# Kernel optimization log

Hardware: AMD Instinct MI355X
Metric: run time of the kernel (lower is better)

Reference implementation:

```python
import jax, jax.numpy as jnp
import numpy as np

EMBED = 768
HEADS = 12
HEAD_DIM = EMBED // HEADS
WINDOW_SIZES = (16, 64, 256)
LN_EPS = 1e-5


def setup_inputs() -> dict:
    key = jax.random.key(0)
    ks = jax.random.split(key, 8)
    B, S = 4, 1024
    s = 1.0 / np.sqrt(EMBED)
    return {
        "query": jax.random.normal(ks[0], (B, S, EMBED), dtype=jnp.float32),
        "key": jax.random.normal(ks[1], (B, S, EMBED), dtype=jnp.float32),
        "value": jax.random.normal(ks[2], (B, S, EMBED), dtype=jnp.float32),
        "attention_mask": jnp.ones((B, S), dtype=jnp.float32),
        "Wq": jax.random.normal(ks[3], (EMBED, EMBED), dtype=jnp.float32) * s,
        "bq": jnp.zeros((EMBED,), dtype=jnp.float32),
        "Wk": jax.random.normal(ks[4], (EMBED, EMBED), dtype=jnp.float32) * s,
        "bk": jnp.zeros((EMBED,), dtype=jnp.float32),
        "Wv": jax.random.normal(ks[5], (EMBED, EMBED), dtype=jnp.float32) * s,
        "bv": jnp.zeros((EMBED,), dtype=jnp.float32),
        "window_weights": jnp.ones((len(WINDOW_SIZES),), dtype=jnp.float32) / len(WINDOW_SIZES),
        "gamma": jnp.ones((EMBED,), dtype=jnp.float32),
        "beta": jnp.zeros((EMBED,), dtype=jnp.float32),
    }


def reference(query, key, value, attention_mask, Wq, bq, Wk, bk, Wv, bv,
              window_weights, gamma, beta):
    B, S, _ = query.shape

    def proj(x, W, b):
        # [B,S,E] -> [B,H,S,D]  (torch nn.Linear: x @ W.T + b)
        return (x @ W.T + b).reshape(B, S, HEADS, HEAD_DIM).transpose(0, 2, 1, 3)

    q = proj(query, Wq, bq)
    k = proj(key, Wk, bk)
    v = proj(value, Wv, bv)

    # full [B,H,S,S] scores (dropout in eval mode = identity)
    scores = jnp.einsum("bhqd,bhkd->bhqk", q, k) / np.sqrt(HEAD_DIM)

    idx = jnp.arange(S)
    am = attention_mask[:, None, None, :]  # broadcast over heads and query dim
    combined = jnp.zeros_like(scores)
    for i, w in enumerate(WINDOW_SIZES):
        # band mask |i-j| <= w; note scores are multiplicatively masked
        # and carried across scales, exactly as in the torch loop
        band = (jnp.abs(idx[:, None] - idx[None, :]) <= w).astype(scores.dtype)
        scores = scores * band * am
        combined = combined + window_weights[i] * jax.nn.softmax(scores, axis=-1)

    context = jnp.einsum("bhqk,bhkd->bhqd", combined, v)
    context = context.transpose(0, 2, 1, 3).reshape(B, S, EMBED)
    q_flat = q.transpose(0, 2, 1, 3).reshape(B, S, EMBED)

    x = q_flat + context
    mean = jnp.mean(x, axis=-1, keepdims=True)
    var = jnp.var(x, axis=-1, keepdims=True)
    return gamma * (x - mean) / jnp.sqrt(var + LN_EPS) + beta
```

## Files before the change

### kernel.cpp

```cpp
#include <hip/hip_runtime.h>
#include <hip/hip_bf16.h>

#define EMB   768
#define SEQ   1024
#define NBAT  4
#define MROWS 4096
#define NHEAD 12
#define HD    64
#define WIN   16
#define QB    16
#define KB    64
#define LN_EPS 1e-5f

typedef __attribute__((ext_vector_type(8))) short bf16x8;
typedef __attribute__((ext_vector_type(4))) float f32x4;
typedef unsigned short u16;
typedef unsigned int   u32;

static __device__ inline u16 f2bf(float f) {
    union { float f; u32 u; } a; a.f = f;
    u32 u = a.u;
    u32 r = (u + 0x7fffu + ((u >> 16) & 1u)) >> 16;
    return (u16)r;
}
static __device__ inline float bf2f(u16 x) {
    union { u32 u; float f; } c; c.u = ((u32)x) << 16; return c.f;
}

#define ACT4 786432u
#define WT4  147456u
__global__ __launch_bounds__(256) void cast_all(
    const float* __restrict__ q, const float* __restrict__ k, const float* __restrict__ v,
    const float* __restrict__ wq, const float* __restrict__ wk, const float* __restrict__ wv,
    u16* __restrict__ Abf, u16* __restrict__ Wbf)
{
    u32 u = blockIdx.x * 256u + threadIdx.x;
    const float* src; u16* dst; u32 off;
    if (u < 3u * ACT4) {
        u32 which = u / ACT4;
        off = (u - which * ACT4) * 4u;
        src = which == 0 ? q : (which == 1 ? k : v);
        dst = Abf + (size_t)which * 3145728u + off;
    } else {
        u32 w2 = u - 3u * ACT4;
        u32 which = w2 / WT4;
        off = (w2 - which * WT4) * 4u;
        src = which == 0 ? wq : (which == 1 ? wk : wv);
        dst = Wbf + (size_t)which * 589824u + off;
    }
    float4 val = *(const float4*)(src + off);
    ushort4 o;
    o.x = f2bf(val.x); o.y = f2bf(val.y); o.z = f2bf(val.z); o.w = f2bf(val.w);
    *(ushort4*)dst = o;
}

#define GK 768
#define GN 768

static __device__ inline void gload_lds16(const void* g, void* l) {
    __builtin_amdgcn_global_load_lds((const __attribute__((address_space(1))) void*)g,
                                     (__attribute__((address_space(3))) void*)l, 16, 0, 0);
}

__global__ __launch_bounds__(256) void gemm_qkv(
    const u16* __restrict__ Abase, const u16* __restrict__ Wbase,
    const float* __restrict__ bq, const float* __restrict__ bk, const float* __restrict__ bv,
    u16* __restrict__ Qb, u16* __restrict__ Kb, u16* __restrict__ Vb)
{
    const int z = blockIdx.z;
    const u16* A = Abase + (size_t)z * (MROWS * GK);
    const u16* W = Wbase + (size_t)z * (GN * GK);
    const float* bias = (z == 0) ? bq : ((z == 1) ? bk : bv);
    u16* Ob = (z == 0) ? Qb : ((z == 1) ? Kb : Vb);

    int id = blockIdx.y * 6 + blockIdx.x;
    int swz = (id & 7) * 48 + (id >> 3);
    const int bm = (swz / 6) * 64, bn = (swz % 6) * 128;

    const int tid = threadIdx.x, wave = tid >> 6, lane = tid & 63;

    __shared__ __align__(16) u16 As[2][64 * 64];
    __shared__ __align__(16) u16 Bs[2][128 * 64];

    f32x4 acc[2][4];
#pragma unroll
    for (int i = 0; i < 2; ++i)
#pragma unroll
        for (int j = 0; j < 4; ++j) acc[i][j] = (f32x4){0.f, 0.f, 0.f, 0.f};

    const int wr = (wave >> 1) * 32, wc = (wave & 1) * 64;
    const int r0 = lane & 15, hk = lane >> 4;

    int arow[2], acol[2], brow[4], bcol[4];
#pragma unroll
    for (int j = 0; j < 2; ++j) {
        int c = j * 256 + tid;
        arow[j] = c >> 3;
        acol[j] = ((c & 7) ^ (arow[j] & 7)) * 8;
    }
#pragma unroll
    for (int j = 0; j < 4; ++j) {
        int c = j * 256 + tid;
        brow[j] = c >> 3;
        bcol[j] = ((c & 7) ^ (brow[j] & 7)) * 8;
    }

#define GEMM_STAGE(buf, K0) do { \
    _Pragma("unroll") for (int j = 0; j < 2; ++j) \
        gload_lds16(A + (size_t)(bm + arow[j]) * GK + (K0) + acol[j], \
                    &As[buf][(j * 256 + wave * 64) * 8]); \
    _Pragma("unroll") for (int j = 0; j < 4; ++j) \
        gload_lds16(W + (size_t)(bn + brow[j]) * GK + (K0) + bcol[j], \
                    &Bs[buf][(j * 256 + wave * 64) * 8]); \
} while (0)

#define GEMM_COMPUTE(buf) do { \
    bf16x8 af[2][2], bg[2][4]; \
    _Pragma("unroll") for (int kk = 0; kk < 2; ++kk) { \
        _Pragma("unroll") for (int i = 0; i < 2; ++i) { \
            int ra = wr + i * 16 + r0; int sa = (kk * 4 + hk) ^ (ra & 7); \
            af[kk][i] = *(const bf16x8*)&As[buf][ra * 64 + sa * 8]; } \
        _Pragma("unroll") for (int j = 0; j < 4; ++j) { \
            int rb = wc + j * 16 + r0; int sb = (kk * 4 + hk) ^ (rb & 7); \
            bg[kk][j] = *(const bf16x8*)&Bs[buf][rb * 64 + sb * 8]; } } \
    _Pragma("unroll") for (int kk = 0; kk < 2; ++kk) \
    _Pragma("unroll") for (int i = 0; i < 2; ++i) \
    _Pragma("unroll") for (int j = 0; j < 4; ++j) \
        acc[i][j] = __builtin_amdgcn_mfma_f32_16x16x32_bf16(af[kk][i], bg[kk][j], acc[i][j], 0, 0, 0); \
} while (0)

    GEMM_STAGE(0, 0);
    for (int t = 0; t < 11; ++t) {
        int cur = t & 1;
        GEMM_STAGE(cur ^ 1, (t + 1) * 64);
        asm volatile("s_waitcnt vmcnt(6)" ::: "memory");
        __builtin_amdgcn_sched_barrier(0);
        __builtin_amdgcn_s_barrier();
        __builtin_amdgcn_sched_barrier(0);
        GEMM_COMPUTE(cur);
        __builtin_amdgcn_sched_barrier(0);
        __builtin_amdgcn_s_barrier();
        __builtin_amdgcn_sched_barrier(0);
    }
    asm volatile("s_waitcnt vmcnt(0)" ::: "memory");
    __builtin_amdgcn_sched_barrier(0);
    __builtin_amdgcn_s_barrier();
    __builtin_amdgcn_sched_barrier(0);
    GEMM_COMPUTE(1);

#undef GEMM_STAGE
#undef GEMM_COMPUTE

    const int cl = lane & 15, rb4 = (lane >> 4) * 4;
#pragma unroll
    for (int i = 0; i < 2; ++i)
#pragma unroll
        for (int j = 0; j < 4; ++j) {
            int col = bn + wc + j * 16 + cl;
            float b_ = bias[col];
#pragma unroll
            for (int r = 0; r < 4; ++r) {
                int row = bm + wr + i * 16 + rb4 + r;
                Ob[(size_t)row * GN + col] = f2bf(acc[i][j][r] + b_);
            }
        }
}

__global__ __launch_bounds__(256) void vsum_kernel(const u16* __restrict__ Vb, float* __restrict__ Vsum)
{
    const int b = blockIdx.y;
    const int l = threadIdx.x & 63, sg = threadIdx.x >> 6;
    const int e = blockIdx.x * 64 + l;
    float s = 0.f;
    const u16* p = Vb + ((size_t)b * SEQ + sg * 256) * EMB + e;
    for (int r = 0; r < 256; ++r) s += bf2f(p[(size_t)r * EMB]);
    __shared__ float red[4][64];
    red[sg][l] = s;
    __syncthreads();
    if (sg == 0) Vsum[b * EMB + e] = red[0][l] + red[1][l] + red[2][l] + red[3][l];
}

__global__ __launch_bounds__(768, 3) void attn_ln(
    const u16* __restrict__ Qb, const u16* __restrict__ Kb, const u16* __restrict__ Vb,
    const float* __restrict__ Vsum, const float* __restrict__ am, const float* __restrict__ ww,
    const float* __restrict__ gamma, const float* __restrict__ beta, float* __restrict__ out)
{
    int id = blockIdx.x + 64 * blockIdx.y;
    int swz = (id & 7) * 32 + (id >> 3);
    const int qt = swz & 63, b = swz >> 6;

    const int q0 = qt * QB;
    int kstart = q0 - WIN;
    if (kstart < 0) kstart = 0;
    if (kstart > SEQ - KB) kstart = SEQ - KB;

    const int h = threadIdx.x >> 6, lane = threadIdx.x & 63;
    const int fr = lane & 15, hk = lane >> 4;
    const int kof = hk * 8, rowg = hk * 4;

    __shared__ __align__(16) u16 Ps[NHEAD][QB][68];
    __shared__ float ps1[QB][13], ps2[QB][13];
    __shared__ float mu[QB], rs[QB];

    const float w0 = ww[0], w1 = ww[1], w2 = ww[2];

    bf16x8 aq[2], bk4[4][2], bv4[4][2];
    {
        const u16* qb = Qb + ((size_t)(b * SEQ + q0)) * EMB + h * HD;
#pragma unroll
        for (int kk = 0; kk < 2; ++kk)
            aq[kk] = *(const bf16x8*)(qb + (size_t)fr * EMB + kk * 32 + kof);
        const u16* kb = Kb + ((size_t)(b * SEQ + kstart)) * EMB + h * HD;
#pragma unroll
        for (int nj = 0; nj < 4; ++nj)
#pragma unroll
            for (int kk = 0; kk < 2; ++kk)
                bk4[nj][kk] = *(const bf16x8*)(kb + (size_t)(nj * 16 + fr) * EMB + kk * 32 + kof);
        const u16* vb = Vb + ((size_t)(b * SEQ + kstart)) * EMB + h * HD;
#pragma unroll
        for (int nj = 0; nj < 4; ++nj)
#pragma unroll
            for (int kk = 0; kk < 2; ++kk) {
                union { bf16x8 v; u16 s[8]; } tmp;
#pragma unroll
                for (int j = 0; j < 8; ++j)
                    tmp.s[j] = vb[(size_t)(kk * 32 + kof + j) * EMB + nj * 16 + fr];
                bv4[nj][kk] = tmp.v;
            }
    }

    f32x4 sc[4];
#pragma unroll
    for (int j = 0; j < 4; ++j) sc[j] = (f32x4){0.f, 0.f, 0.f, 0.f};
#pragma unroll
    for (int kk = 0; kk < 2; ++kk)
#pragma unroll
        for (int nj = 0; nj < 4; ++nj)
            sc[nj] = __builtin_amdgcn_mfma_f32_16x16x32_bf16(aq[kk], bk4[nj][kk], sc[nj], 0, 0, 0);

    float amv[4];
#pragma unroll
    for (int nj = 0; nj < 4; ++nj) amv[nj] = am[b * SEQ + kstart + nj * 16 + fr];

    float t[4][4], cj[4][4], ua[4];
#pragma unroll
    for (int nj = 0; nj < 4; ++nj)
#pragma unroll
        for (int r = 0; r < 4; ++r) {
            int qrow = q0 + rowg + r;
            int kcol = kstart + nj * 16 + fr;
            int d = qrow - kcol; if (d < 0) d = -d;
            t[nj][r] = (d <= WIN) ? sc[nj][r] * 0.125f * amv[nj] : 0.f;
            cj[nj][r] = 0.f;
        }
#pragma unroll
    for (int r = 0; r < 4; ++r) ua[r] = 0.f;

#pragma unroll
    for (int it = 0; it < 3; ++it) {
        float wwi = it == 0 ? w0 : (it == 1 ? w1 : w2);
#pragma unroll
        for (int r = 0; r < 4; ++r) {
            float m = 0.f;
#pragma unroll
            for (int nj = 0; nj < 4; ++nj) m = fmaxf(m, t[nj][r]);
#pragma unroll
            for (int o = 1; o < 16; o <<= 1) m = fmaxf(m, __shfl_xor(m, o, 64));
            float e4[4], s = 0.f;
#pragma unroll
            for (int nj = 0; nj < 4; ++nj) { e4[nj] = __expf(t[nj][r] - m); s += e4[nj]; }
#pragma unroll
            for (int o = 1; o < 16; o <<= 1) s += __shfl_xor(s, o, 64);
            float un = __expf(-m);
            s += (float)(SEQ - KB) * un;
            float inv = wwi / s;
#pragma unroll
            for (int nj = 0; nj < 4; ++nj) cj[nj][r] += e4[nj] * inv;
            ua[r] += un * inv;
        }
        if (it < 2) {
#pragma unroll
            for (int nj = 0; nj < 4; ++nj)
#pragma unroll
                for (int r = 0; r < 4; ++r) t[nj][r] *= amv[nj];
        }
    }

#pragma unroll
    for (int nj = 0; nj < 4; ++nj)
#pragma unroll
        for (int r = 0; r < 4; ++r)
            Ps[h][rowg + r][nj * 16 + fr] = f2bf(cj[nj][r] - ua[r]);

    f32x4 pv[4];
#pragma unroll
    for (int j = 0; j < 4; ++j) pv[j] = (f32x4){0.f, 0.f, 0.f, 0.f};
#pragma unroll
    for (int kk = 0; kk < 2; ++kk) {
        bf16x8 ap = *(const bf16x8*)&Ps[h][fr][kk * 32 + kof];
#pragma unroll
        for (int nj = 0; nj < 4; ++nj)
            pv[nj] = __builtin_amdgcn_mfma_f32_16x16x32_bf16(ap, bv4[nj][kk], pv[nj], 0, 0, 0);
    }

    float vs[4];
#pragma unroll
    for (int nj = 0; nj < 4; ++nj) vs[nj] = Vsum[b * EMB + h * HD + nj * 16 + fr];

    float xv[4][4];
#pragma unroll
    for (int nj = 0; nj < 4; ++nj)
#pragma unroll
        for (int r = 0; r < 4; ++r) {
            int row = q0 + rowg + r;
            float qres = bf2f(Qb[((size_t)(b * SEQ + row)) * EMB + h * HD + nj * 16 + fr]);
            xv[nj][r] = qres + pv[nj][r] + ua[r] * vs[nj];
        }

    float s1r[4], s2r[4];
#pragma unroll
    for (int r = 0; r < 4; ++r) {
        float a = 0.f, c = 0.f;
#pragma unroll
        for (int nj = 0; nj < 4; ++nj) { a += xv[nj][r]; c += xv[nj][r] * xv[nj][r]; }
#pragma unroll
        for (int o = 1; o < 16; o <<= 1) { a += __shfl_xor(a, o, 64); c += __shfl_xor(c, o, 64); }
        s1r[r] = a; s2r[r] = c;
    }
    if (fr == 0) {
#pragma unroll
        for (int r = 0; r < 4; ++r) { ps1[rowg + r][h] = s1r[r]; ps2[rowg + r][h] = s2r[r]; }
    }
    __syncthreads();
    if (h == 0 && lane < QB) {
        float a = 0.f, c = 0.f;
#pragma unroll
        for (int w = 0; w < NHEAD; ++w) { a += ps1[lane][w]; c += ps2[lane][w]; }
        float mean = a * (1.f / EMB);
        float var = c * (1.f / EMB) - mean * mean;
        mu[lane] = mean;
        rs[lane] = rsqrtf(var + LN_EPS);
    }
    __syncthreads();

#pragma unroll
    for (int nj = 0; nj < 4; ++nj) {
        int col = h * HD + nj * 16 + fr;
        float g = gamma[col], be = beta[col];
#pragma unroll
        for (int r = 0; r < 4; ++r) {
            int row = q0 + rowg + r;
            out[((size_t)(b * SEQ + row)) * EMB + col] =
                g * (xv[nj][r] - mu[rowg + r]) * rs[rowg + r] + be;
        }
    }
}

extern "C" void kernel_launch(void* const* d_in, const int* in_sizes, int n_in,
                              void* d_out, int out_size, void* d_ws, size_t ws_size,
                              hipStream_t stream)
{
    const float* q     = (const float*)d_in[0];
    const float* k     = (const float*)d_in[1];
    const float* v     = (const float*)d_in[2];
    const float* amask = (const float*)d_in[3];
    const float* Wq    = (const float*)d_in[4];
    const float* bq    = (const float*)d_in[5];
    const float* Wk    = (const float*)d_in[6];
    const float* bk    = (const float*)d_in[7];
    const float* Wv    = (const float*)d_in[8];
    const float* bv    = (const float*)d_in[9];
    const float* ww    = (const float*)d_in[10];
    const float* gamma = (const float*)d_in[11];
    const float* beta  = (const float*)d_in[12];
    float* out = (float*)d_out;

    char* ws = (char*)d_ws;
    u16*   Abf  = (u16*)(ws);
    u16*   Wbf  = (u16*)(ws + 18874368);
    u16*   Qbf  = (u16*)(ws + 22413312);
    u16*   Kbf  = (u16*)(ws + 28704768);
    u16*   Vbf  = (u16*)(ws + 34996224);
    float* Vsum = (float*)(ws + 41287680);

    hipLaunchKernelGGL(cast_all, dim3(10944), dim3(256), 0, stream,
                       q, k, v, Wq, Wk, Wv, Abf, Wbf);
    hipLaunchKernelGGL(gemm_qkv, dim3(GN / 128, MROWS / 64, 3), dim3(256), 0, stream,
                       Abf, Wbf, bq, bk, bv, Qbf, Kbf, Vbf);
    hipLaunchKernelGGL(vsum_kernel, dim3(EMB / 64, NBAT), dim3(256), 0, stream,
                       Vbf, Vsum);
    hipLaunchKernelGGL(attn_ln, dim3(SEQ / QB, NBAT), dim3(768), 0, stream,
                       Qbf, Kbf, Vbf, Vsum, amask, ww, gamma, beta, out);
}
```

Before: 65.97 us.

## Fuse activation bf16 cast into QKV GEMM and pre-transpose V for attention

Drops the separate cast pass over the fp32 query/key/value activations. The GEMM now loads fp32 A fragments straight from global memory into registers, converts them to bf16 and feeds MFMA directly, while W still goes through LDS via async loads. The vsum kernel also writes a transposed copy of V so the attention kernel can load V fragments with vector loads instead of strided scalar gathers. The trade-offs are twice the A-side global bytes per GEMM block, no LDS reuse of A across waves, and an extra V-sized write.

```diff
diff --git a/kernel.cpp b/kernel.cpp
--- a/kernel.cpp
+++ b/kernel.cpp
@@ -26,32 +26,30 @@
 static __device__ inline float bf2f(u16 x) {
     union { u32 u; float f; } c; c.u = ((u32)x) << 16; return c.f;
 }
-
-#define ACT4 786432u
+static __device__ inline u32 cvt2(float lo, float hi) {
+    __hip_bfloat162 t = __float22bfloat162_rn(float2{lo, hi});
+    union { __hip_bfloat162 h; u32 u; } c; c.h = t; return c.u;
+}
+static __device__ inline bf16x8 pack8(float4 a, float4 b) {
+    union { bf16x8 v; u32 w[4]; } r;
+    r.w[0] = cvt2(a.x, a.y); r.w[1] = cvt2(a.z, a.w);
+    r.w[2] = cvt2(b.x, b.y); r.w[3] = cvt2(b.z, b.w);
+    return r.v;
+}
+
 #define WT4  147456u
-__global__ __launch_bounds__(256) void cast_all(
-    const float* __restrict__ q, const float* __restrict__ k, const float* __restrict__ v,
+__global__ __launch_bounds__(256) void cast_w(
     const float* __restrict__ wq, const float* __restrict__ wk, const float* __restrict__ wv,
-    u16* __restrict__ Abf, u16* __restrict__ Wbf)
+    u16* __restrict__ Wbf)
 {
     u32 u = blockIdx.x * 256u + threadIdx.x;
-    const float* src; u16* dst; u32 off;
-    if (u < 3u * ACT4) {
-        u32 which = u / ACT4;
-        off = (u - which * ACT4) * 4u;
-        src = which == 0 ? q : (which == 1 ? k : v);
-        dst = Abf + (size_t)which * 3145728u + off;
-    } else {
-        u32 w2 = u - 3u * ACT4;
-        u32 which = w2 / WT4;
-        off = (w2 - which * WT4) * 4u;
-        src = which == 0 ? wq : (which == 1 ? wk : wv);
-        dst = Wbf + (size_t)which * 589824u + off;
-    }
+    u32 which = u / WT4;
+    u32 off = (u - which * WT4) * 4u;
+    const float* src = which == 0 ? wq : (which == 1 ? wk : wv);
     float4 val = *(const float4*)(src + off);
     ushort4 o;
     o.x = f2bf(val.x); o.y = f2bf(val.y); o.z = f2bf(val.z); o.w = f2bf(val.w);
-    *(ushort4*)dst = o;
+    *(ushort4*)(Wbf + (size_t)which * 589824u + off) = o;
 }
 
 #define GK 768
@@ -63,12 +61,13 @@
 }
 
 __global__ __launch_bounds__(256) void gemm_qkv(
-    const u16* __restrict__ Abase, const u16* __restrict__ Wbase,
+    const float* __restrict__ qa, const float* __restrict__ ka, const float* __restrict__ va,
+    const u16* __restrict__ Wbase,
     const float* __restrict__ bq, const float* __restrict__ bk, const float* __restrict__ bv,
     u16* __restrict__ Qb, u16* __restrict__ Kb, u16* __restrict__ Vb)
 {
     const int z = blockIdx.z;
-    const u16* A = Abase + (size_t)z * (MROWS * GK);
+    const float* Af = (z == 0) ? qa : ((z == 1) ? ka : va);
     const u16* W = Wbase + (size_t)z * (GN * GK);
     const float* bias = (z == 0) ? bq : ((z == 1) ? bk : bv);
     u16* Ob = (z == 0) ? Qb : ((z == 1) ? Kb : Vb);
@@ -79,7 +78,6 @@
 
     const int tid = threadIdx.x, wave = tid >> 6, lane = tid & 63;
 
-    __shared__ __align__(16) u16 As[2][64 * 64];
     __shared__ __align__(16) u16 Bs[2][128 * 64];
 
     f32x4 acc[2][4];
@@ -90,14 +88,12 @@
 
     const int wr = (wave >> 1) * 32, wc = (wave & 1) * 64;
     const int r0 = lane & 15, hk = lane >> 4;
-
-    int arow[2], acol[2], brow[4], bcol[4];
-#pragma unroll
-    for (int j = 0; j < 2; ++j) {
-        int c = j * 256 + tid;
-        arow[j] = c >> 3;
-        acol[j] = ((c & 7) ^ (arow[j] & 7)) * 8;
-    }
+    const int fr = r0, kof = hk * 8;
+
+    const float* a0 = Af + (size_t)(bm + wr + fr) * GK + kof;
+    const float* a1 = a0 + 16 * GK;
+
+    int brow[4], bcol[4];
 #pragma unroll
     for (int j = 0; j < 4; ++j) {
         int c = j * 256 + tid;
@@ -105,35 +101,53 @@
         bcol[j] = ((c & 7) ^ (brow[j] & 7)) * 8;
     }
 
-#define GEMM_STAGE(buf, K0) do { \
-    _Pragma("unroll") for (int j = 0; j < 2; ++j) \
-        gload_lds16(A + (size_t)(bm + arow[j]) * GK + (K0) + acol[j], \
-                    &As[buf][(j * 256 + wave * 64) * 8]); \
+    float4 raw[2][2][2];
+    bf16x8 afrag[2][2];
+
+#define B_STAGE(buf, K0) do { \
     _Pragma("unroll") for (int j = 0; j < 4; ++j) \
         gload_lds16(W + (size_t)(bn + brow[j]) * GK + (K0) + bcol[j], \
                     &Bs[buf][(j * 256 + wave * 64) * 8]); \
 } while (0)
 
+#define ARAW(T) do { int kb = (T) * 64; \
+    raw[0][0][0] = *(const float4*)(a0 + kb);      raw[0][0][1] = *(const float4*)(a0 + kb + 4); \
+    raw[0][1][0] = *(const float4*)(a0 + kb + 32); raw[0][1][1] = *(const float4*)(a0 + kb + 36); \
+    raw[1][0][0] = *(const float4*)(a1 + kb);      raw[1][0][1] = *(const float4*)(a1 + kb + 4); \
+    raw[1][1][0] = *(const float4*)(a1 + kb + 32); raw[1][1][1] = *(const float4*)(a1 + kb + 36); \
+} while (0)
+
+#define ACVT() do { \
+    _Pragma("unroll") for (int kk = 0; kk < 2; ++kk) \
+    _Pragma("unroll") for (int i = 0; i < 2; ++i) \
+        afrag[kk][i] = pack8(raw[i][kk][0], raw[i][kk][1]); \
+} while (0)
+
 #define GEMM_COMPUTE(buf) do { \
-    bf16x8 af[2][2], bg[2][4]; \
-    _Pragma("unroll") for (int kk = 0; kk < 2; ++kk) { \
-        _Pragma("unroll") for (int i = 0; i < 2; ++i) { \
-            int ra = wr + i * 16 + r0; int sa = (kk * 4 + hk) ^ (ra & 7); \
-            af[kk][i] = *(const bf16x8*)&As[buf][ra * 64 + sa * 8]; } \
-        _Pragma("unroll") for (int j = 0; j < 4; ++j) { \
-            int rb = wc + j * 16 + r0; int sb = (kk * 4 + hk) ^ (rb & 7); \
-            bg[kk][j] = *(const bf16x8*)&Bs[buf][rb * 64 + sb * 8]; } } \
+    bf16x8 bg[2][4]; \
+    _Pragma("unroll") for (int kk = 0; kk < 2; ++kk) \
+    _Pragma("unroll") for (int j = 0; j < 4; ++j) { \
+        int rb = wc + j * 16 + r0; int sb = (kk * 4 + hk) ^ (rb & 7); \
+        bg[kk][j] = *(const bf16x8*)&Bs[buf][rb * 64 + sb * 8]; } \
     _Pragma("unroll") for (int kk = 0; kk < 2; ++kk) \
     _Pragma("unroll") for (int i = 0; i < 2; ++i) \
     _Pragma("unroll") for (int j = 0; j < 4; ++j) \
-        acc[i][j] = __builtin_amdgcn_mfma_f32_16x16x32_bf16(af[kk][i], bg[kk][j], acc[i][j], 0, 0, 0); \
+        acc[i][j] = __builtin_amdgcn_mfma_f32_16x16x32_bf16(afrag[kk][i], bg[kk][j], acc[i][j], 0, 0, 0); \
 } while (0)
 
-    GEMM_STAGE(0, 0);
-    for (int t = 0; t < 11; ++t) {
+    B_STAGE(0, 0);
+    ARAW(0);
+    for (int t = 0; t < 12; ++t) {
         int cur = t & 1;
-        GEMM_STAGE(cur ^ 1, (t + 1) * 64);
-        asm volatile("s_waitcnt vmcnt(6)" ::: "memory");
+        if (t < 11) {
+            B_STAGE(cur ^ 1, (t + 1) * 64);
+            asm volatile("s_waitcnt vmcnt(4)" ::: "memory");
+        } else {
+            asm volatile("s_waitcnt vmcnt(0)" ::: "memory");
+        }
+        __builtin_amdgcn_sched_barrier(0);
+        ACVT();
+        if (t < 11) ARAW(t + 1);
         __builtin_amdgcn_sched_barrier(0);
         __builtin_amdgcn_s_barrier();
         __builtin_amdgcn_sched_barrier(0);
@@ -142,13 +156,10 @@
         __builtin_amdgcn_s_barrier();
         __builtin_amdgcn_sched_barrier(0);
     }
-    asm volatile("s_waitcnt vmcnt(0)" ::: "memory");
-    __builtin_amdgcn_sched_barrier(0);
-    __builtin_amdgcn_s_barrier();
-    __builtin_amdgcn_sched_barrier(0);
-    GEMM_COMPUTE(1);
-
-#undef GEMM_STAGE
+
+#undef B_STAGE
+#undef ARAW
+#undef ACVT
 #undef GEMM_COMPUTE
 
     const int cl = lane & 15, rb4 = (lane >> 4) * 4;
@@ -166,14 +177,26 @@
         }
 }
 
-__global__ __launch_bounds__(256) void vsum_kernel(const u16* __restrict__ Vb, float* __restrict__ Vsum)
+__global__ __launch_bounds__(256) void vsum_kernel(const u16* __restrict__ Vb,
+                                                   float* __restrict__ Vsum,
+                                                   u16* __restrict__ Vt)
 {
     const int b = blockIdx.y;
     const int l = threadIdx.x & 63, sg = threadIdx.x >> 6;
     const int e = blockIdx.x * 64 + l;
     float s = 0.f;
     const u16* p = Vb + ((size_t)b * SEQ + sg * 256) * EMB + e;
-    for (int r = 0; r < 256; ++r) s += bf2f(p[(size_t)r * EMB]);
+    u16* vt = Vt + ((size_t)(b * EMB + e)) * SEQ + sg * 256;
+    for (int r8 = 0; r8 < 32; ++r8) {
+        union { bf16x8 v; u16 s8[8]; } buf;
+#pragma unroll
+        for (int j = 0; j < 8; ++j) {
+            u16 val = p[(size_t)(r8 * 8 + j) * EMB];
+            s += bf2f(val);
+            buf.s8[j] = val;
+        }
+        *(bf16x8*)(vt + r8 * 8) = buf.v;
+    }
     __shared__ float red[4][64];
     red[sg][l] = s;
     __syncthreads();
@@ -181,7 +204,7 @@
 }
 
 __global__ __launch_bounds__(768, 3) void attn_ln(
-    const u16* __restrict__ Qb, const u16* __restrict__ Kb, const u16* __restrict__ Vb,
+    const u16* __restrict__ Qb, const u16* __restrict__ Kb, const u16* __restrict__ Vt,
     const float* __restrict__ Vsum, const float* __restrict__ am, const float* __restrict__ ww,
     const float* __restrict__ gamma, const float* __restrict__ beta, float* __restrict__ out)
 {
@@ -216,17 +239,12 @@
 #pragma unroll
             for (int kk = 0; kk < 2; ++kk)
                 bk4[nj][kk] = *(const bf16x8*)(kb + (size_t)(nj * 16 + fr) * EMB + kk * 32 + kof);
-        const u16* vb = Vb + ((size_t)(b * SEQ + kstart)) * EMB + h * HD;
+        const u16* vt = Vt + ((size_t)(b * EMB + h * HD)) * SEQ + kstart;
 #pragma unroll
         for (int nj = 0; nj < 4; ++nj)
 #pragma unroll
-            for (int kk = 0; kk < 2; ++kk) {
-                union { bf16x8 v; u16 s[8]; } tmp;
-#pragma unroll
-                for (int j = 0; j < 8; ++j)
-                    tmp.s[j] = vb[(size_t)(kk * 32 + kof + j) * EMB + nj * 16 + fr];
-                bv4[nj][kk] = tmp.v;
-            }
+            for (int kk = 0; kk < 2; ++kk)
+                bv4[nj][kk] = *(const bf16x8*)(vt + (size_t)(nj * 16 + fr) * SEQ + kk * 32 + kof);
     }
 
     f32x4 sc[4];
@@ -376,19 +394,19 @@
     float* out = (float*)d_out;
 
     char* ws = (char*)d_ws;
-    u16*   Abf  = (u16*)(ws);
-    u16*   Wbf  = (u16*)(ws + 18874368);
-    u16*   Qbf  = (u16*)(ws + 22413312);
-    u16*   Kbf  = (u16*)(ws + 28704768);
-    u16*   Vbf  = (u16*)(ws + 34996224);
-    float* Vsum = (float*)(ws + 41287680);
-
-    hipLaunchKernelGGL(cast_all, dim3(10944), dim3(256), 0, stream,
-                       q, k, v, Wq, Wk, Wv, Abf, Wbf);
+    u16*   Wbf  = (u16*)(ws);
+    u16*   Qbf  = (u16*)(ws + 3538944);
+    u16*   Kbf  = (u16*)(ws + 9830400);
+    u16*   Vbf  = (u16*)(ws + 16121856);
+    u16*   Vt   = (u16*)(ws + 22413312);
+    float* Vsum = (float*)(ws + 28704768);
+
+    hipLaunchKernelGGL(cast_w, dim3(1728), dim3(256), 0, stream,
+                       Wq, Wk, Wv, Wbf);
     hipLaunchKernelGGL(gemm_qkv, dim3(GN / 128, MROWS / 64, 3), dim3(256), 0, stream,
-                       Abf, Wbf, bq, bk, bv, Qbf, Kbf, Vbf);
+                       q, k, v, Wbf, bq, bk, bv, Qbf, Kbf, Vbf);
     hipLaunchKernelGGL(vsum_kernel, dim3(EMB / 64, NBAT), dim3(256), 0, stream,
-                       Vbf, Vsum);
+                       Vbf, Vsum, Vt);
     hipLaunchKernelGGL(attn_ln, dim3(SEQ / QB, NBAT), dim3(768), 0, stream,
-                       Qbf, Kbf, Vbf, Vsum, amask, ww, gamma, beta, out);
-}
+                       Qbf, Kbf, Vt, Vsum, amask, ww, gamma, beta, out);
+}
```

Result: slower. 107.6 us (+63.2%).
